# Performance work log

Measured on AMD Instinct MI355X. Metric: run time of the kernel, lower is better.

## Reference

```python
import jax, jax.numpy as jnp
import numpy as np

GRID_SIZE = 64
THRESHOLD = 1.0
SIGMA = 1.5
K_SHARP = 2.0


def _gaussian_kernel(sigma):
    ksize = max(int(4 * sigma) | 1, 3)
    x = jnp.arange(ksize, dtype=jnp.float32) - ksize // 2
    g1d = jnp.exp(-x ** 2 / (2.0 * sigma ** 2))
    g2d = g1d[None, :] * g1d[:, None]
    g2d = g2d / g2d.sum()
    return g2d[None, None]  # (1,1,k,k) OIHW


def setup_inputs() -> dict:
    key = jax.random.key(0)
    k1, k2, k3, k4 = jax.random.split(key, 4)
    B, V, P, N, MAXP = 4, 512, 8192, 2000, 8
    positions = jax.random.uniform(k1, (B, V, 2), dtype=jnp.float32) * 2.0 - 1.0
    pin_offsets = jax.random.normal(k2, (P, 2), dtype=jnp.float32) * 0.05
    net_to_pin = jax.random.randint(k3, (N, MAXP), 0, P, dtype=jnp.int32)
    pin_to_macro = jax.random.randint(k4, (P,), 0, V, dtype=jnp.int32)
    return {"positions": positions, "pin_offsets": pin_offsets,
            "net_to_pin": net_to_pin, "pin_to_macro": pin_to_macro}


def reference(positions, pin_offsets, net_to_pin, pin_to_macro):
    B = positions.shape[0]
    M = GRID_SIZE
    num_nets = net_to_pin.shape[0]

    # pin positions: (B, P, 2) -- no rotation (rotation_onehot=None branch)
    pin_pos = positions[:, pin_to_macro, :] + pin_offsets[None]

    # per-net bounding boxes over valid pins
    valid = net_to_pin >= 0                                  # (N, maxp)
    safe_idx = jnp.maximum(net_to_pin, 0)
    net_pin_pos = pin_pos[:, safe_idx, :]                    # (B, N, maxp, 2)
    mask = valid[None, :, :, None]
    bbox_max = jnp.max(jnp.where(mask, net_pin_pos, -1e9), axis=2)  # (B, N, 2)
    bbox_min = jnp.min(jnp.where(mask, net_pin_pos, 1e9), axis=2)

    # to grid coordinates
    bbox_max_g = (bbox_max + 1.0) * 0.5 * (M - 1)
    bbox_min_g = (bbox_min + 1.0) * 0.5 * (M - 1)

    # soft rectangular indicators on the MxM grid
    gx = jnp.arange(M, dtype=jnp.float32)
    grid_x, grid_y = jnp.meshgrid(gx, gx, indexing="xy")     # (M, M)
    grid_x = grid_x[None, None]                               # (1,1,M,M)
    grid_y = grid_y[None, None]
    x_min = bbox_min_g[..., 0][..., None, None]               # (B,N,1,1)
    x_max = bbox_max_g[..., 0][..., None, None]
    y_min = bbox_min_g[..., 1][..., None, None]
    y_max = bbox_max_g[..., 1][..., None, None]

    in_x = jax.nn.sigmoid(K_SHARP * (grid_x - x_min + 0.5)) * \
           jax.nn.sigmoid(K_SHARP * (x_max - grid_x + 0.5))
    in_y = jax.nn.sigmoid(K_SHARP * (grid_y - y_min + 0.5)) * \
           jax.nn.sigmoid(K_SHARP * (y_max - grid_y + 0.5))
    indicator = in_x * in_y                                    # (B,N,M,M)

    bbox_size = jnp.maximum((x_max - x_min + 1.0) * (y_max - y_min + 1.0), 1.0)
    rudy = jnp.sum(indicator / bbox_size, axis=1, keepdims=True)  # (B,1,M,M)

    # gaussian smoothing (SAME padding)
    kernel = _gaussian_kernel(SIGMA)
    pad = kernel.shape[-1] // 2
    rudy_smooth = jax.lax.conv_general_dilated(
        rudy, kernel, window_strides=(1, 1),
        padding=((pad, pad), (pad, pad)),
        dimension_numbers=("NCHW", "OIHW", "NCHW"))

    overflow = jax.nn.relu(rudy_smooth - THRESHOLD)
    penalty = jnp.sum(overflow ** 2, axis=(1, 2, 3))           # (B,)
    return penalty, rudy_smooth
```

## Files before the change

### kernel.cpp

```cpp
#include <hip/hip_runtime.h>

#define GRID   64
#define BATCH  4
#define NV     512
#define NP     8192
#define NNET   2000
#define MAXPIN 8
#define NB     32
#define NCHUNK 63
#define CELLS  (GRID * GRID)

__device__ __forceinline__ float sigmoidf_fast(float z) {
    return 1.0f / (1.0f + __expf(-z));
}

__global__ __launch_bounds__(256)
void rudy_partial_kernel(const float* __restrict__ positions,
                         const float* __restrict__ pin_offsets,
                         const int*   __restrict__ net_to_pin,
                         const int*   __restrict__ pin_to_macro,
                         float* __restrict__ partial) {
    const int chunk = blockIdx.x;
    const int b     = blockIdx.y;
    const int t     = threadIdx.x;

    __shared__ float s_inx[NB][GRID];
    __shared__ float s_iny[NB][GRID];
    __shared__ float s_xmin[NB], s_xmax[NB], s_ymin[NB], s_ymax[NB], s_inv[NB];

    {
        const int nl = t >> 3;
        const int j  = t & 7;
        const int n  = chunk * NB + nl;
        int pi = (n < NNET) ? net_to_pin[n * MAXPIN + j] : -1;
        int sp = pi > 0 ? pi : 0;
        int v  = pin_to_macro[sp];
        float px = positions[(b * NV + v) * 2 + 0] + pin_offsets[sp * 2 + 0];
        float py = positions[(b * NV + v) * 2 + 1] + pin_offsets[sp * 2 + 1];
        bool valid = pi >= 0;
        float xmx = valid ? px : -1e9f;
        float xmn = valid ? px :  1e9f;
        float ymx = valid ? py : -1e9f;
        float ymn = valid ? py :  1e9f;
        #pragma unroll
        for (int off = 1; off < 8; off <<= 1) {
            xmx = fmaxf(xmx, __shfl_xor(xmx, off, 64));
            xmn = fminf(xmn, __shfl_xor(xmn, off, 64));
            ymx = fmaxf(ymx, __shfl_xor(ymx, off, 64));
            ymn = fminf(ymn, __shfl_xor(ymn, off, 64));
        }
        if (j == 0) {
            float xming = (xmn + 1.0f) * 31.5f;
            float xmaxg = (xmx + 1.0f) * 31.5f;
            float yming = (ymn + 1.0f) * 31.5f;
            float ymaxg = (ymx + 1.0f) * 31.5f;
            float size = fmaxf((xmaxg - xming + 1.0f) * (ymaxg - yming + 1.0f), 1.0f);
            s_xmin[nl] = xming; s_xmax[nl] = xmaxg;
            s_ymin[nl] = yming; s_ymax[nl] = ymaxg;
            s_inv[nl]  = 1.0f / size;
        }
    }
    __syncthreads();

    #pragma unroll
    for (int i = 0; i < 16; ++i) {
        int v     = i * 256 + t;
        int n     = v >> 7;
        int rem   = v & 127;
        int which = rem >> 6;
        int coord = rem & 63;
        float c  = (float)coord;
        float lo = which ? s_ymin[n] : s_xmin[n];
        float hi = which ? s_ymax[n] : s_xmax[n];
        float val = sigmoidf_fast(2.0f * (c - lo + 0.5f)) *
                    sigmoidf_fast(2.0f * (hi - c + 0.5f));
        if (which) s_iny[n][coord] = val; else s_inx[n][coord] = val;
    }
    __syncthreads();

    const int lane = t & 63;
    const int w    = t >> 6;
    float acc[16];
    #pragma unroll
    for (int k = 0; k < 16; ++k) acc[k] = 0.0f;

    for (int n = 0; n < NB; ++n) {
        float xv = s_inx[n][lane] * s_inv[n];
        const float4* iny4 = (const float4*)&s_iny[n][w * 16];
        #pragma unroll
        for (int k4 = 0; k4 < 4; ++k4) {
            float4 yv = iny4[k4];
            acc[k4 * 4 + 0] += yv.x * xv;
            acc[k4 * 4 + 1] += yv.y * xv;
            acc[k4 * 4 + 2] += yv.z * xv;
            acc[k4 * 4 + 3] += yv.w * xv;
        }
    }

    float* dst = partial + (b * NCHUNK + chunk) * CELLS;
    #pragma unroll
    for (int k = 0; k < 16; ++k) {
        dst[(w * 16 + k) * GRID + lane] = acc[k];
    }
}

__global__ __launch_bounds__(1024)
void smooth_penalty_kernel(const float* __restrict__ partial,
                           float* __restrict__ out_penalty,
                           float* __restrict__ out_smooth) {
    const int b = blockIdx.x;
    const int t = threadIdx.x;

    __shared__ float tile[CELLS];
    __shared__ float tmp [CELLS];
    __shared__ float red[16];

    float g[7];
    {
        float s = 0.0f;
        #pragma unroll
        for (int i = 0; i < 7; ++i) {
            float d = (float)(i - 3);
            g[i] = expf(-d * d / 4.5f);
            s += g[i];
        }
        float inv = 1.0f / s;
        #pragma unroll
        for (int i = 0; i < 7; ++i) g[i] *= inv;
    }

    const float* base = partial + b * NCHUNK * CELLS;
    float sum[4] = {0.0f, 0.0f, 0.0f, 0.0f};
    for (int ch = 0; ch < NCHUNK; ++ch) {
        const float* p = base + ch * CELLS;
        #pragma unroll
        for (int k = 0; k < 4; ++k) sum[k] += p[k * 1024 + t];
    }
    #pragma unroll
    for (int k = 0; k < 4; ++k) tile[k * 1024 + t] = sum[k];
    __syncthreads();

    #pragma unroll
    for (int k = 0; k < 4; ++k) {
        int c = k * 1024 + t;
        int y = c >> 6, x = c & 63;
        float s = 0.0f;
        #pragma unroll
        for (int d = -3; d <= 3; ++d) {
            int xx = x + d;
            if (xx >= 0 && xx < GRID) s += g[d + 3] * tile[y * GRID + xx];
        }
        tmp[c] = s;
    }
    __syncthreads();

    float local = 0.0f;
    #pragma unroll
    for (int k = 0; k < 4; ++k) {
        int c = k * 1024 + t;
        int y = c >> 6, x = c & 63;
        float s = 0.0f;
        #pragma unroll
        for (int d = -3; d <= 3; ++d) {
            int yy = y + d;
            if (yy >= 0 && yy < GRID) s += g[d + 3] * tmp[yy * GRID + x];
        }
        out_smooth[b * CELLS + c] = s;
        float ov = s - 1.0f;
        ov = ov > 0.0f ? ov : 0.0f;
        local += ov * ov;
    }

    #pragma unroll
    for (int off = 32; off > 0; off >>= 1) local += __shfl_down(local, off, 64);
    if ((t & 63) == 0) red[t >> 6] = local;
    __syncthreads();
    if (t == 0) {
        float s = 0.0f;
        #pragma unroll
        for (int i = 0; i < 16; ++i) s += red[i];
        out_penalty[b] = s;
    }
}

extern "C" void kernel_launch(void* const* d_in, const int* in_sizes, int n_in,
                              void* d_out, int out_size, void* d_ws, size_t ws_size,
                              hipStream_t stream) {
    const float* positions    = (const float*)d_in[0];
    const float* pin_offsets  = (const float*)d_in[1];
    const int*   net_to_pin   = (const int*)d_in[2];
    const int*   pin_to_macro = (const int*)d_in[3];
    float* out     = (float*)d_out;
    float* partial = (float*)d_ws;

    rudy_partial_kernel<<<dim3(NCHUNK, BATCH), 256, 0, stream>>>(
        positions, pin_offsets, net_to_pin, pin_to_macro, partial);
    smooth_penalty_kernel<<<BATCH, 1024, 0, stream>>>(partial, out, out + BATCH);
}
```

Baseline: 81.95 us.

## Use fewer, larger net chunks and vectorize the partial-sum reduction

```diff
diff --git a/kernel.cpp b/kernel.cpp
--- a/kernel.cpp
+++ b/kernel.cpp
@@ -6,8 +6,8 @@
 #define NP     8192
 #define NNET   2000
 #define MAXPIN 8
-#define NB     32
-#define NCHUNK 63
+#define NB     125
+#define NCHUNK 16
 #define CELLS  (GRID * GRID)
 
 __device__ __forceinline__ float sigmoidf_fast(float z) {
@@ -28,53 +28,54 @@
     __shared__ float s_iny[NB][GRID];
     __shared__ float s_xmin[NB], s_xmax[NB], s_ymin[NB], s_ymax[NB], s_inv[NB];
 
-    {
-        const int nl = t >> 3;
-        const int j  = t & 7;
-        const int n  = chunk * NB + nl;
-        int pi = (n < NNET) ? net_to_pin[n * MAXPIN + j] : -1;
-        int sp = pi > 0 ? pi : 0;
-        int v  = pin_to_macro[sp];
-        float px = positions[(b * NV + v) * 2 + 0] + pin_offsets[sp * 2 + 0];
-        float py = positions[(b * NV + v) * 2 + 1] + pin_offsets[sp * 2 + 1];
-        bool valid = pi >= 0;
-        float xmx = valid ? px : -1e9f;
-        float xmn = valid ? px :  1e9f;
-        float ymx = valid ? py : -1e9f;
-        float ymn = valid ? py :  1e9f;
-        #pragma unroll
-        for (int off = 1; off < 8; off <<= 1) {
-            xmx = fmaxf(xmx, __shfl_xor(xmx, off, 64));
-            xmn = fminf(xmn, __shfl_xor(xmn, off, 64));
-            ymx = fmaxf(ymx, __shfl_xor(ymx, off, 64));
-            ymn = fminf(ymn, __shfl_xor(ymn, off, 64));
-        }
-        if (j == 0) {
-            float xming = (xmn + 1.0f) * 31.5f;
-            float xmaxg = (xmx + 1.0f) * 31.5f;
-            float yming = (ymn + 1.0f) * 31.5f;
-            float ymaxg = (ymx + 1.0f) * 31.5f;
-            float size = fmaxf((xmaxg - xming + 1.0f) * (ymaxg - yming + 1.0f), 1.0f);
-            s_xmin[nl] = xming; s_xmax[nl] = xmaxg;
-            s_ymin[nl] = yming; s_ymax[nl] = ymaxg;
-            s_inv[nl]  = 1.0f / size;
-        }
-    }
-    __syncthreads();
-
-    #pragma unroll
-    for (int i = 0; i < 16; ++i) {
-        int v     = i * 256 + t;
-        int n     = v >> 7;
-        int rem   = v & 127;
-        int which = rem >> 6;
-        int coord = rem & 63;
-        float c  = (float)coord;
-        float lo = which ? s_ymin[n] : s_xmin[n];
-        float hi = which ? s_ymax[n] : s_xmax[n];
-        float val = sigmoidf_fast(2.0f * (c - lo + 0.5f)) *
-                    sigmoidf_fast(2.0f * (hi - c + 0.5f));
-        if (which) s_iny[n][coord] = val; else s_inx[n][coord] = val;
+    if (t < NB) {
+        const int n = chunk * NB + t;
+        const int4* np4 = (const int4*)(net_to_pin + n * MAXPIN);
+        int4 q0 = np4[0], q1 = np4[1];
+        int pis[8] = {q0.x, q0.y, q0.z, q0.w, q1.x, q1.y, q1.z, q1.w};
+        float xmn = 1e9f, xmx = -1e9f, ymn = 1e9f, ymx = -1e9f;
+        const float2* pos2 = (const float2*)positions;
+        const float2* off2 = (const float2*)pin_offsets;
+        #pragma unroll
+        for (int j = 0; j < MAXPIN; ++j) {
+            int pi = pis[j];
+            int sp = pi > 0 ? pi : 0;
+            int v  = pin_to_macro[sp];
+            float2 p = pos2[b * NV + v];
+            float2 o = off2[sp];
+            float px = p.x + o.x, py = p.y + o.y;
+            bool valid = pi >= 0;
+            float vx_hi = valid ? px : -1e9f, vx_lo = valid ? px : 1e9f;
+            float vy_hi = valid ? py : -1e9f, vy_lo = valid ? py : 1e9f;
+            xmx = fmaxf(xmx, vx_hi); xmn = fminf(xmn, vx_lo);
+            ymx = fmaxf(ymx, vy_hi); ymn = fminf(ymn, vy_lo);
+        }
+        float xming = (xmn + 1.0f) * 31.5f;
+        float xmaxg = (xmx + 1.0f) * 31.5f;
+        float yming = (ymn + 1.0f) * 31.5f;
+        float ymaxg = (ymx + 1.0f) * 31.5f;
+        float size = fmaxf((xmaxg - xming + 1.0f) * (ymaxg - yming + 1.0f), 1.0f);
+        s_xmin[t] = xming; s_xmax[t] = xmaxg;
+        s_ymin[t] = yming; s_ymax[t] = ymaxg;
+        s_inv[t]  = 1.0f / size;
+    }
+    __syncthreads();
+
+    #pragma unroll
+    for (int i = 0; i < 63; ++i) {
+        int v = i * 256 + t;
+        if (v < NB * 128) {
+            int n     = v >> 7;
+            int rem   = v & 127;
+            int which = rem >> 6;
+            int coord = rem & 63;
+            float c  = (float)coord;
+            float lo = which ? s_ymin[n] : s_xmin[n];
+            float hi = which ? s_ymax[n] : s_xmax[n];
+            float val = sigmoidf_fast(2.0f * (c - lo + 0.5f)) *
+                        sigmoidf_fast(2.0f * (hi - c + 0.5f));
+            if (which) s_iny[n][coord] = val; else s_inx[n][coord] = val;
+        }
     }
     __syncthreads();
 
@@ -84,6 +85,7 @@
     #pragma unroll
     for (int k = 0; k < 16; ++k) acc[k] = 0.0f;
 
+    #pragma unroll 5
     for (int n = 0; n < NB; ++n) {
         float xv = s_inx[n][lane] * s_inv[n];
         const float4* iny4 = (const float4*)&s_iny[n][w * 16];
@@ -129,15 +131,14 @@
         for (int i = 0; i < 7; ++i) g[i] *= inv;
     }
 
-    const float* base = partial + b * NCHUNK * CELLS;
-    float sum[4] = {0.0f, 0.0f, 0.0f, 0.0f};
+    const float4* base4 = (const float4*)(partial + b * NCHUNK * CELLS);
+    float4 s4 = make_float4(0.0f, 0.0f, 0.0f, 0.0f);
+    #pragma unroll
     for (int ch = 0; ch < NCHUNK; ++ch) {
-        const float* p = base + ch * CELLS;
-        #pragma unroll
-        for (int k = 0; k < 4; ++k) sum[k] += p[k * 1024 + t];
-    }
-    #pragma unroll
-    for (int k = 0; k < 4; ++k) tile[k * 1024 + t] = sum[k];
+        float4 v = base4[ch * 1024 + t];
+        s4.x += v.x; s4.y += v.y; s4.z += v.z; s4.w += v.w;
+    }
+    ((float4*)tile)[t] = s4;
     __syncthreads();
 
     #pragma unroll
```

After: 80.94 us. Within noise of the previous version (-1.2%).
